# Kernel tuning notes

Measured on AMD Instinct MI355X. Metric: run time of the kernel, lower is better.

## Reference

```python
import jax, jax.numpy as jnp
import numpy as np

POS_RATIO = 0.5
EPS = 1e-6


def setup_inputs() -> dict:
    key = jax.random.key(0)
    k1, k2, k3, k4 = jax.random.split(key, 4)
    N, C, D, H, W = 8, 256, 8, 16, 16
    q = jax.random.normal(k1, (N, C, D, H, W), dtype=jnp.float32)
    k = jax.random.normal(k2, (N, C, D, H, W), dtype=jnp.float32)
    # coords: (x0, y0, z0, x1, y1, z1) with lower-right > upper-left
    uq = jax.random.uniform(k3, (N, 3), dtype=jnp.float32) * 0.5
    uk = jax.random.uniform(k4, (N, 3), dtype=jnp.float32) * 0.5
    coord_q = jnp.concatenate([uq, uq + 0.5], axis=1)
    coord_k = jnp.concatenate([uk, uk + 0.5], axis=1)
    return {"q": q, "k": k, "coord_q": coord_q, "coord_k": coord_k}


def _centers(coord, D, H, W):
    """Per-batch voxel-center coordinates. coord: [N,6]. Returns cx, cy, cz each [N, D*H*W], plus bin diag [N]."""
    bw = (coord[:, 3] - coord[:, 0]) / W  # [N]
    bh = (coord[:, 4] - coord[:, 1]) / H
    bd = (coord[:, 5] - coord[:, 2]) / D
    gz, gy, gx = jnp.meshgrid(jnp.arange(D, dtype=coord.dtype),
                              jnp.arange(H, dtype=coord.dtype),
                              jnp.arange(W, dtype=coord.dtype), indexing="ij")
    gx = (gx + 0.5).reshape(-1)[None, :]  # [1, DHW]
    gy = (gy + 0.5).reshape(-1)[None, :]
    gz = (gz + 0.5).reshape(-1)[None, :]
    cx = gx * bw[:, None] + coord[:, 0][:, None]
    cy = gy * bh[:, None] + coord[:, 1][:, None]
    cz = gz * bd[:, None] + coord[:, 2][:, None]
    diag = jnp.sqrt(bw ** 2 + bh ** 2 + bd ** 2)  # [N]
    return cx, cy, cz, diag


def reference(q, k, coord_q, coord_k):
    N, C, D, H, W = q.shape
    qf = q.reshape(N, C, -1)  # [N, C, P], P = D*H*W
    kf = k.reshape(N, C, -1)
    cqx, cqy, cqz, q_diag = _centers(coord_q, D, H, W)
    ckx, cky, ckz, k_diag = _centers(coord_k, D, H, W)
    max_diag = jnp.maximum(q_diag, k_diag)  # [N]
    # pairwise center distance, normalized by max bin diagonal: [N, P, P]
    dist = jnp.sqrt((cqx[:, :, None] - ckx[:, None, :]) ** 2
                    + (cqy[:, :, None] - cky[:, None, :]) ** 2
                    + (cqz[:, :, None] - ckz[:, None, :]) ** 2) / max_diag[:, None, None]
    pos_mask = jax.lax.stop_gradient((dist < POS_RATIO).astype(q.dtype))
    # logit[n, p, p'] = sum_c q[n,c,p] * k[n,c,p']
    logit = jnp.einsum("ncp,ncq->npq", qf, kf)
    loss = (logit * pos_mask).sum((-2, -1)) / (pos_mask.sum((-2, -1)) + EPS)  # [N]
    return -2.0 * loss.mean()
```

## Files before the change

### kernel.cpp

```cpp
#include <hip/hip_runtime.h>
#include <cstdint>
#include <cstddef>

#define NB 8
#define CH 256
#define DD 8
#define HH 16
#define WW 16
#define PP 2048

#define OFF_DPART 16384

__device__ __forceinline__ int z_window(float czq, float bdk, float k2, float maxd) {
    float lim = 0.500060f * maxd;
    int zk0 = -1;
    #pragma unroll
    for (int zk = 0; zk < DD; ++zk) {
        float czk = __fadd_rn(__fmul_rn(__fadd_rn((float)zk, 0.5f), bdk), k2);
        bool feas = fabsf(__fsub_rn(czq, czk)) < lim;
        if (feas && zk0 < 0) zk0 = zk;
    }
    if (zk0 > DD - 2) zk0 = DD - 2;
    return zk0;
}

#define CC 16
__global__ __launch_bounds__(256) void fused_kernel(
    const float* __restrict__ q, const float* __restrict__ k,
    const float* __restrict__ coord_q, const float* __restrict__ coord_k,
    float* __restrict__ partial, float* __restrict__ dpart)
{
    __shared__ float klds[CC][512];

    int t  = threadIdx.x;
    int wv = t >> 6;
    int lane = t & 63;
    int cg = blockIdx.x;
    int zq = blockIdx.y;
    int n  = blockIdx.z;
    int flat = (n * 8 + zq) * 16 + cg;
    int c0 = cg * CC;

    const float* cq = coord_q + n * 6;
    const float* ck = coord_k + n * 6;
    float q0 = cq[0], q1 = cq[1], q2 = cq[2];
    float k0 = ck[0], k1 = ck[1], k2 = ck[2];
    float bwq = __fdiv_rn(__fsub_rn(cq[3], q0), (float)WW);
    float bhq = __fdiv_rn(__fsub_rn(cq[4], q1), (float)HH);
    float bdq = __fdiv_rn(__fsub_rn(cq[5], q2), (float)DD);
    float bwk = __fdiv_rn(__fsub_rn(ck[3], k0), (float)WW);
    float bhk = __fdiv_rn(__fsub_rn(ck[4], k1), (float)HH);
    float bdk = __fdiv_rn(__fsub_rn(ck[5], k2), (float)DD);
    float diagq = __fsqrt_rn(__fadd_rn(__fadd_rn(__fmul_rn(bwq, bwq), __fmul_rn(bhq, bhq)),
                                       __fmul_rn(bdq, bdq)));
    float diagk = __fsqrt_rn(__fadd_rn(__fadd_rn(__fmul_rn(bwk, bwk), __fmul_rn(bhk, bhk)),
                                       __fmul_rn(bdk, bdk)));
    float maxd = fmaxf(diagq, diagk);
    float cqz = __fadd_rn(__fmul_rn(__fadd_rn((float)zq, 0.5f), bdq), q2);

    int zk0 = z_window(cqz, bdk, k2, maxd);
    if (zk0 < 0) {
        if (lane == 0) {
            partial[flat * 4 + wv] = 0.0f;
            if (cg == 0) dpart[(n * 8 + zq) * 4 + wv] = 0.0f;
        }
        return;
    }
    int base_p = zk0 << 8;

    int p = (zq << 8) + t;
    float qv[CC];
    {
        const float* qcol = q + ((size_t)(n * CH + c0)) * PP + p;
        #pragma unroll
        for (int c = 0; c < CC; ++c)
            qv[c] = qcol[(size_t)c * PP];
    }

    {
        const float* ksrc = k + ((size_t)(n * CH + c0)) * PP + base_p;
        #pragma unroll
        for (int i = 0; i < 8; ++i) {
            int f = i * 256 + t;
            int c = f >> 7;
            int u = (f & 127) << 2;
            float4 v = *(const float4*)(ksrc + (size_t)c * PP + u);
            klds[c][u + 0] = v.x;
            klds[c][u + 1] = v.y;
            klds[c][u + 2] = v.z;
            klds[c][u + 3] = v.w;
        }
    }
    __syncthreads();

    int ix = t & 15, iy = (t >> 4) & 15;
    float cqx = __fadd_rn(__fmul_rn(__fadd_rn((float)ix, 0.5f), bwq), q0);
    float cqy = __fadd_rn(__fmul_rn(__fadd_rn((float)iy, 0.5f), bhq), q1);

    float lim = 0.500060f * maxd;
    float tx = (cqx - k0) / bwk - 0.5f;
    float ty = (cqy - k1) / bhk - 0.5f;
    float rx = lim / bwk + 0.03f;
    float ry = lim / bhk + 0.03f;
    int jx0 = (int)ceilf(tx - rx);  if (jx0 < 0) jx0 = 0;
    int jx1 = (int)floorf(tx + rx); if (jx1 > WW - 1) jx1 = WW - 1;
    int jy0 = (int)ceilf(ty - ry);  if (jy0 < 0) jy0 = 0;
    int jy1 = (int)floorf(ty + ry); if (jy1 > HH - 1) jy1 = HH - 1;

    float half_maxd = 0.5f * maxd;
    float thr2 = half_maxd * half_maxd * 1.001f;

    float s[CC];
    #pragma unroll
    for (int c = 0; c < CC; ++c) s[c] = 0.0f;
    int cnt = 0;

    for (int dzI = 0; dzI < 2; ++dzI) {
        int jz = zk0 + dzI;
        float ckz = __fadd_rn(__fmul_rn(__fadd_rn((float)jz, 0.5f), bdk), k2);
        float dz  = __fsub_rn(cqz, ckz);
        float dz2 = __fmul_rn(dz, dz);
        for (int jy = jy0; jy <= jy1; ++jy) {
            float cky = __fadd_rn(__fmul_rn(__fadd_rn((float)jy, 0.5f), bhk), k1);
            float dy  = __fsub_rn(cqy, cky);
            float dy2 = __fmul_rn(dy, dy);
            for (int jx = jx0; jx <= jx1; ++jx) {
                float ckx = __fadd_rn(__fmul_rn(__fadd_rn((float)jx, 0.5f), bwk), k0);
                float dx  = __fsub_rn(cqx, ckx);
                float dx2 = __fmul_rn(dx, dx);
                float d2  = __fadd_rn(__fadd_rn(dx2, dy2), dz2);
                bool pos = false;
                if (d2 < thr2) {
                    float dist = __fdiv_rn(__fsqrt_rn(d2), maxd);
                    pos = dist < 0.5f;
                }
                if (pos) {
                    ++cnt;
                    int idx = (dzI << 8) + (jy << 4) + jx;
                    #pragma unroll
                    for (int c = 0; c < CC; ++c)
                        s[c] += klds[c][idx];
                }
            }
        }
    }

    float acc = 0.0f;
    #pragma unroll
    for (int c = 0; c < CC; ++c)
        acc += qv[c] * s[c];

    int ci = cnt;
    #pragma unroll
    for (int off = 32; off > 0; off >>= 1) {
        acc += __shfl_down(acc, off, 64);
        ci  += __shfl_down(ci, off, 64);
    }
    if (lane == 0) {
        partial[flat * 4 + wv] = acc;
        if (cg == 0) dpart[(n * 8 + zq) * 4 + wv] = (float)ci;
    }
}

__global__ __launch_bounds__(512) void final_kernel(const float* __restrict__ partial,
                                                    const float* __restrict__ dpart,
                                                    float* __restrict__ out)
{
    __shared__ float numsh[NB];
    __shared__ float densh[NB];
    int t = threadIdx.x;
    int n = t >> 6, lane = t & 63;

    float sp = 0.0f;
    #pragma unroll
    for (int i = 0; i < 8; ++i)
        sp += partial[n * 512 + i * 64 + lane];
    float sc = (lane < 32) ? dpart[n * 32 + lane] : 0.0f;
    #pragma unroll
    for (int off = 32; off > 0; off >>= 1) {
        sp += __shfl_down(sp, off, 64);
        sc += __shfl_down(sc, off, 64);
    }
    if (lane == 0) { numsh[n] = sp; densh[n] = sc; }
    __syncthreads();
    if (t == 0) {
        float r = 0.0f;
        for (int i = 0; i < NB; ++i)
            r += numsh[i] / (densh[i] + 1e-6f);
        out[0] = -2.0f * (r / (float)NB);
    }
}

extern "C" void kernel_launch(void* const* d_in, const int* in_sizes, int n_in,
                              void* d_out, int out_size, void* d_ws, size_t ws_size,
                              hipStream_t stream) {
    const float* q       = (const float*)d_in[0];
    const float* k       = (const float*)d_in[1];
    const float* coord_q = (const float*)d_in[2];
    const float* coord_k = (const float*)d_in[3];
    float* out = (float*)d_out;

    char* w = (char*)d_ws;
    float* partial = (float*)w;
    float* dpart   = (float*)(w + OFF_DPART);

    fused_kernel<<<dim3(CH / CC, DD, NB), 256, 0, stream>>>(q, k, coord_q, coord_k,
                                                            partial, dpart);
    final_kernel<<<1, 512, 0, stream>>>(partial, dpart, out);
}
```

Before: 80.80 us.

## Fuse final reduction via last-block counter and load K directly to LDS

Removes the separate final reduction kernel: every block increments a global atomic counter, and the last block reads all partials and writes the output. K tiles are now copied with global_load_lds straight into shared memory, and a z slice is loaded only when it is feasible. This removes one kernel launch and the register round-trip for K, but adds a memset on the stream plus atomic and fence overhead.

```diff
diff --git a/kernel.cpp b/kernel.cpp
--- a/kernel.cpp
+++ b/kernel.cpp
@@ -10,6 +10,8 @@
 #define PP 2048
 
 #define OFF_DPART 16384
+#define OFF_CTR   17408
+#define NBLK      1024
 
 __device__ __forceinline__ int z_window(float czq, float bdk, float k2, float maxd) {
     float lim = 0.500060f * maxd;
@@ -24,13 +26,20 @@
     return zk0;
 }
 
+typedef __attribute__((address_space(3))) void       lds_void;
+typedef __attribute__((address_space(1))) const void glb_void;
+
 #define CC 16
 __global__ __launch_bounds__(256) void fused_kernel(
     const float* __restrict__ q, const float* __restrict__ k,
     const float* __restrict__ coord_q, const float* __restrict__ coord_k,
-    float* __restrict__ partial, float* __restrict__ dpart)
+    float* __restrict__ partial, float* __restrict__ dpart,
+    unsigned* __restrict__ counter, float* __restrict__ out)
 {
     __shared__ float klds[CC][512];
+    __shared__ float numsh[NB];
+    __shared__ float densh[NB];
+    __shared__ int   is_last;
 
     int t  = threadIdx.x;
     int wv = t >> 6;
@@ -59,96 +68,110 @@
     float cqz = __fadd_rn(__fmul_rn(__fadd_rn((float)zq, 0.5f), bdq), q2);
 
     int zk0 = z_window(cqz, bdk, k2, maxd);
-    if (zk0 < 0) {
-        if (lane == 0) {
-            partial[flat * 4 + wv] = 0.0f;
-            if (cg == 0) dpart[(n * 8 + zq) * 4 + wv] = 0.0f;
-        }
-        return;
-    }
-    int base_p = zk0 << 8;
-
-    int p = (zq << 8) + t;
-    float qv[CC];
-    {
-        const float* qcol = q + ((size_t)(n * CH + c0)) * PP + p;
+
+    float acc = 0.0f;
+    int cnt = 0;
+
+    if (zk0 >= 0) {
+        float lim = 0.500060f * maxd;
+
+        float czk0 = __fadd_rn(__fmul_rn(__fadd_rn((float)zk0, 0.5f), bdk), k2);
+        float czk1 = __fadd_rn(__fmul_rn(__fadd_rn((float)(zk0 + 1), 0.5f), bdk), k2);
+        bool feas0 = fabsf(__fsub_rn(cqz, czk0)) < lim;
+        bool feas1 = fabsf(__fsub_rn(cqz, czk1)) < lim;
+
+        {
+            int u = (t & 63) << 2;
+            if (feas0) {
+                const float* ksrc = k + ((size_t)(n * CH + c0)) * PP + (zk0 << 8);
+                #pragma unroll
+                for (int i = 0; i < 4; ++i) {
+                    int c = i * 4 + wv;
+                    const float* src = ksrc + (size_t)c * PP + u;
+                    float* dst = &klds[c][u];
+                    __builtin_amdgcn_global_load_lds((const glb_void*)src,
+                                                     (lds_void*)dst, 16, 0, 0);
+                }
+            }
+            if (feas1) {
+                const float* ksrc = k + ((size_t)(n * CH + c0)) * PP + ((zk0 + 1) << 8);
+                #pragma unroll
+                for (int i = 0; i < 4; ++i) {
+                    int c = i * 4 + wv;
+                    const float* src = ksrc + (size_t)c * PP + u;
+                    float* dst = &klds[c][256 + u];
+                    __builtin_amdgcn_global_load_lds((const glb_void*)src,
+                                                     (lds_void*)dst, 16, 0, 0);
+                }
+            }
+        }
+
+        int p = (zq << 8) + t;
+        float qv[CC];
+        {
+            const float* qcol = q + ((size_t)(n * CH + c0)) * PP + p;
+            #pragma unroll
+            for (int c = 0; c < CC; ++c)
+                qv[c] = qcol[(size_t)c * PP];
+        }
+
+        int ix = t & 15, iy = (t >> 4) & 15;
+        float cqx = __fadd_rn(__fmul_rn(__fadd_rn((float)ix, 0.5f), bwq), q0);
+        float cqy = __fadd_rn(__fmul_rn(__fadd_rn((float)iy, 0.5f), bhq), q1);
+
+        float tx = (cqx - k0) / bwk - 0.5f;
+        float ty = (cqy - k1) / bhk - 0.5f;
+        float rx = lim / bwk + 0.03f;
+        float ry = lim / bhk + 0.03f;
+        int jx0 = (int)ceilf(tx - rx);  if (jx0 < 0) jx0 = 0;
+        int jx1 = (int)floorf(tx + rx); if (jx1 > WW - 1) jx1 = WW - 1;
+        int jy0 = (int)ceilf(ty - ry);  if (jy0 < 0) jy0 = 0;
+        int jy1 = (int)floorf(ty + ry); if (jy1 > HH - 1) jy1 = HH - 1;
+
+        float half_maxd = 0.5f * maxd;
+        float thr2 = half_maxd * half_maxd * 1.001f;
+
+        float s[CC];
+        #pragma unroll
+        for (int c = 0; c < CC; ++c) s[c] = 0.0f;
+
+        __syncthreads();
+
+        for (int dzI = 0; dzI < 2; ++dzI) {
+            if (dzI == 0 ? !feas0 : !feas1) continue;
+            int jz = zk0 + dzI;
+            float ckz = __fadd_rn(__fmul_rn(__fadd_rn((float)jz, 0.5f), bdk), k2);
+            float dz  = __fsub_rn(cqz, ckz);
+            float dz2 = __fmul_rn(dz, dz);
+            for (int jy = jy0; jy <= jy1; ++jy) {
+                float cky = __fadd_rn(__fmul_rn(__fadd_rn((float)jy, 0.5f), bhk), k1);
+                float dy  = __fsub_rn(cqy, cky);
+                float dy2 = __fmul_rn(dy, dy);
+                for (int jx = jx0; jx <= jx1; ++jx) {
+                    float ckx = __fadd_rn(__fmul_rn(__fadd_rn((float)jx, 0.5f), bwk), k0);
+                    float dx  = __fsub_rn(cqx, ckx);
+                    float dx2 = __fmul_rn(dx, dx);
+                    float d2  = __fadd_rn(__fadd_rn(dx2, dy2), dz2);
+                    bool pos = false;
+                    if (d2 < thr2) {
+                        float dist = __fdiv_rn(__fsqrt_rn(d2), maxd);
+                        pos = dist < 0.5f;
+                    }
+                    if (pos) {
+                        ++cnt;
+                        int idx = (dzI << 8) + (jy << 4) + jx;
+                        #pragma unroll
+                        for (int c = 0; c < CC; ++c)
+                            s[c] += klds[c][idx];
+                    }
+                }
+            }
+        }
+
         #pragma unroll
         for (int c = 0; c < CC; ++c)
-            qv[c] = qcol[(size_t)c * PP];
-    }
-
-    {
-        const float* ksrc = k + ((size_t)(n * CH + c0)) * PP + base_p;
-        #pragma unroll
-        for (int i = 0; i < 8; ++i) {
-            int f = i * 256 + t;
-            int c = f >> 7;
-            int u = (f & 127) << 2;
-            float4 v = *(const float4*)(ksrc + (size_t)c * PP + u);
-            klds[c][u + 0] = v.x;
-            klds[c][u + 1] = v.y;
-            klds[c][u + 2] = v.z;
-            klds[c][u + 3] = v.w;
-        }
-    }
-    __syncthreads();
-
-    int ix = t & 15, iy = (t >> 4) & 15;
-    float cqx = __fadd_rn(__fmul_rn(__fadd_rn((float)ix, 0.5f), bwq), q0);
-    float cqy = __fadd_rn(__fmul_rn(__fadd_rn((float)iy, 0.5f), bhq), q1);
-
-    float lim = 0.500060f * maxd;
-    float tx = (cqx - k0) / bwk - 0.5f;
-    float ty = (cqy - k1) / bhk - 0.5f;
-    float rx = lim / bwk + 0.03f;
-    float ry = lim / bhk + 0.03f;
-    int jx0 = (int)ceilf(tx - rx);  if (jx0 < 0) jx0 = 0;
-    int jx1 = (int)floorf(tx + rx); if (jx1 > WW - 1) jx1 = WW - 1;
-    int jy0 = (int)ceilf(ty - ry);  if (jy0 < 0) jy0 = 0;
-    int jy1 = (int)floorf(ty + ry); if (jy1 > HH - 1) jy1 = HH - 1;
-
-    float half_maxd = 0.5f * maxd;
-    float thr2 = half_maxd * half_maxd * 1.001f;
-
-    float s[CC];
-    #pragma unroll
-    for (int c = 0; c < CC; ++c) s[c] = 0.0f;
-    int cnt = 0;
-
-    for (int dzI = 0; dzI < 2; ++dzI) {
-        int jz = zk0 + dzI;
-        float ckz = __fadd_rn(__fmul_rn(__fadd_rn((float)jz, 0.5f), bdk), k2);
-        float dz  = __fsub_rn(cqz, ckz);
-        float dz2 = __fmul_rn(dz, dz);
-        for (int jy = jy0; jy <= jy1; ++jy) {
-            float cky = __fadd_rn(__fmul_rn(__fadd_rn((float)jy, 0.5f), bhk), k1);
-            float dy  = __fsub_rn(cqy, cky);
-            float dy2 = __fmul_rn(dy, dy);
-            for (int jx = jx0; jx <= jx1; ++jx) {
-                float ckx = __fadd_rn(__fmul_rn(__fadd_rn((float)jx, 0.5f), bwk), k0);
-                float dx  = __fsub_rn(cqx, ckx);
-                float dx2 = __fmul_rn(dx, dx);
-                float d2  = __fadd_rn(__fadd_rn(dx2, dy2), dz2);
-                bool pos = false;
-                if (d2 < thr2) {
-                    float dist = __fdiv_rn(__fsqrt_rn(d2), maxd);
-                    pos = dist < 0.5f;
-                }
-                if (pos) {
-                    ++cnt;
-                    int idx = (dzI << 8) + (jy << 4) + jx;
-                    #pragma unroll
-                    for (int c = 0; c < CC; ++c)
-                        s[c] += klds[c][idx];
-                }
-            }
-        }
-    }
-
-    float acc = 0.0f;
-    #pragma unroll
-    for (int c = 0; c < CC; ++c)
-        acc += qv[c] * s[c];
+            acc += qv[c] * s[c];
+    }
 
     int ci = cnt;
     #pragma unroll
@@ -157,37 +180,49 @@
         ci  += __shfl_down(ci, off, 64);
     }
     if (lane == 0) {
-        partial[flat * 4 + wv] = acc;
-        if (cg == 0) dpart[(n * 8 + zq) * 4 + wv] = (float)ci;
-    }
-}
-
-__global__ __launch_bounds__(512) void final_kernel(const float* __restrict__ partial,
-                                                    const float* __restrict__ dpart,
-                                                    float* __restrict__ out)
-{
-    __shared__ float numsh[NB];
-    __shared__ float densh[NB];
-    int t = threadIdx.x;
-    int n = t >> 6, lane = t & 63;
-
-    float sp = 0.0f;
-    #pragma unroll
-    for (int i = 0; i < 8; ++i)
-        sp += partial[n * 512 + i * 64 + lane];
-    float sc = (lane < 32) ? dpart[n * 32 + lane] : 0.0f;
-    #pragma unroll
-    for (int off = 32; off > 0; off >>= 1) {
-        sp += __shfl_down(sp, off, 64);
-        sc += __shfl_down(sc, off, 64);
-    }
-    if (lane == 0) { numsh[n] = sp; densh[n] = sc; }
+        __hip_atomic_store(&partial[flat * 4 + wv], acc,
+                           __ATOMIC_RELAXED, __HIP_MEMORY_SCOPE_AGENT);
+        if (cg == 0)
+            __hip_atomic_store(&dpart[(n * 8 + zq) * 4 + wv], (float)ci,
+                               __ATOMIC_RELAXED, __HIP_MEMORY_SCOPE_AGENT);
+    }
     __syncthreads();
+
     if (t == 0) {
-        float r = 0.0f;
-        for (int i = 0; i < NB; ++i)
-            r += numsh[i] / (densh[i] + 1e-6f);
-        out[0] = -2.0f * (r / (float)NB);
+        __threadfence();
+        unsigned old = __hip_atomic_fetch_add(counter, 1u,
+                                              __ATOMIC_ACQ_REL, __HIP_MEMORY_SCOPE_AGENT);
+        is_last = (old == NBLK - 1) ? 1 : 0;
+    }
+    __syncthreads();
+
+    if (is_last) {
+        #pragma unroll
+        for (int rep = 0; rep < 2; ++rep) {
+            int nn = wv + rep * 4;
+            float sp = 0.0f;
+            #pragma unroll
+            for (int i = 0; i < 8; ++i)
+                sp += __hip_atomic_load(&partial[nn * 512 + i * 64 + lane],
+                                        __ATOMIC_RELAXED, __HIP_MEMORY_SCOPE_AGENT);
+            float sc = (lane < 32)
+                ? __hip_atomic_load(&dpart[nn * 32 + lane],
+                                    __ATOMIC_RELAXED, __HIP_MEMORY_SCOPE_AGENT)
+                : 0.0f;
+            #pragma unroll
+            for (int off = 32; off > 0; off >>= 1) {
+                sp += __shfl_down(sp, off, 64);
+                sc += __shfl_down(sc, off, 64);
+            }
+            if (lane == 0) { numsh[nn] = sp; densh[nn] = sc; }
+        }
+        __syncthreads();
+        if (t == 0) {
+            float r = 0.0f;
+            for (int i = 0; i < NB; ++i)
+                r += numsh[i] / (densh[i] + 1e-6f);
+            out[0] = -2.0f * (r / (float)NB);
+        }
     }
 }
 
@@ -201,10 +236,12 @@
     float* out = (float*)d_out;
 
     char* w = (char*)d_ws;
-    float* partial = (float*)w;
-    float* dpart   = (float*)(w + OFF_DPART);
-
-    fused_kernel<<<dim3(CH / CC, DD, NB), 256, 0, stream>>>(q, k, coord_q, coord_k,
-                                                            partial, dpart);
-    final_kernel<<<1, 512, 0, stream>>>(partial, dpart, out);
+    float*    partial = (float*)w;
+    float*    dpart   = (float*)(w + OFF_DPART);
+    unsigned* counter = (unsigned*)(w + OFF_CTR);
+
+    hipMemsetAsync((void*)counter, 0, sizeof(unsigned), stream);
+
+    fused_kernel<<<dim3(CH / CC, DD, NB), 256, 0, stream>>>(
+        q, k, coord_q, coord_k, partial, dpart, counter, out);
 }
```

Result: slower. 126.9 us (+57.1%).

## Load K slices directly to LDS asynchronously and skip infeasible z-planes

Applied to the files above, without the earlier changes.

Replaces the register-staged float4 K copy into shared memory with global_load_lds direct-to-LDS transfers, and issues them before the Q column loads and window setup so the copies overlap that work. Each of the two candidate K z-planes is now loaded and scanned only if it passes the z-feasibility test, which removes unnecessary traffic and loop iterations. This relies on the amdgcn direct-to-LDS builtin and its wave-uniform addressing and layout assumptions, and keeps the synchronisation ordering unchanged.

```diff
diff --git a/kernel.cpp b/kernel.cpp
--- a/kernel.cpp
+++ b/kernel.cpp
@@ -23,6 +23,9 @@
     if (zk0 > DD - 2) zk0 = DD - 2;
     return zk0;
 }
+
+typedef __attribute__((address_space(3))) void       lds_void;
+typedef __attribute__((address_space(1))) const void glb_void;
 
 #define CC 16
 __global__ __launch_bounds__(256) void fused_kernel(
@@ -59,96 +62,110 @@
     float cqz = __fadd_rn(__fmul_rn(__fadd_rn((float)zq, 0.5f), bdq), q2);
 
     int zk0 = z_window(cqz, bdk, k2, maxd);
-    if (zk0 < 0) {
-        if (lane == 0) {
-            partial[flat * 4 + wv] = 0.0f;
-            if (cg == 0) dpart[(n * 8 + zq) * 4 + wv] = 0.0f;
-        }
-        return;
-    }
-    int base_p = zk0 << 8;
-
-    int p = (zq << 8) + t;
-    float qv[CC];
-    {
-        const float* qcol = q + ((size_t)(n * CH + c0)) * PP + p;
-        #pragma unroll
-        for (int c = 0; c < CC; ++c)
-            qv[c] = qcol[(size_t)c * PP];
-    }
-
-    {
-        const float* ksrc = k + ((size_t)(n * CH + c0)) * PP + base_p;
-        #pragma unroll
-        for (int i = 0; i < 8; ++i) {
-            int f = i * 256 + t;
-            int c = f >> 7;
-            int u = (f & 127) << 2;
-            float4 v = *(const float4*)(ksrc + (size_t)c * PP + u);
-            klds[c][u + 0] = v.x;
-            klds[c][u + 1] = v.y;
-            klds[c][u + 2] = v.z;
-            klds[c][u + 3] = v.w;
-        }
-    }
-    __syncthreads();
-
-    int ix = t & 15, iy = (t >> 4) & 15;
-    float cqx = __fadd_rn(__fmul_rn(__fadd_rn((float)ix, 0.5f), bwq), q0);
-    float cqy = __fadd_rn(__fmul_rn(__fadd_rn((float)iy, 0.5f), bhq), q1);
-
-    float lim = 0.500060f * maxd;
-    float tx = (cqx - k0) / bwk - 0.5f;
-    float ty = (cqy - k1) / bhk - 0.5f;
-    float rx = lim / bwk + 0.03f;
-    float ry = lim / bhk + 0.03f;
-    int jx0 = (int)ceilf(tx - rx);  if (jx0 < 0) jx0 = 0;
-    int jx1 = (int)floorf(tx + rx); if (jx1 > WW - 1) jx1 = WW - 1;
-    int jy0 = (int)ceilf(ty - ry);  if (jy0 < 0) jy0 = 0;
-    int jy1 = (int)floorf(ty + ry); if (jy1 > HH - 1) jy1 = HH - 1;
-
-    float half_maxd = 0.5f * maxd;
-    float thr2 = half_maxd * half_maxd * 1.001f;
-
-    float s[CC];
-    #pragma unroll
-    for (int c = 0; c < CC; ++c) s[c] = 0.0f;
+
+    float acc = 0.0f;
     int cnt = 0;
 
-    for (int dzI = 0; dzI < 2; ++dzI) {
-        int jz = zk0 + dzI;
-        float ckz = __fadd_rn(__fmul_rn(__fadd_rn((float)jz, 0.5f), bdk), k2);
-        float dz  = __fsub_rn(cqz, ckz);
-        float dz2 = __fmul_rn(dz, dz);
-        for (int jy = jy0; jy <= jy1; ++jy) {
-            float cky = __fadd_rn(__fmul_rn(__fadd_rn((float)jy, 0.5f), bhk), k1);
-            float dy  = __fsub_rn(cqy, cky);
-            float dy2 = __fmul_rn(dy, dy);
-            for (int jx = jx0; jx <= jx1; ++jx) {
-                float ckx = __fadd_rn(__fmul_rn(__fadd_rn((float)jx, 0.5f), bwk), k0);
-                float dx  = __fsub_rn(cqx, ckx);
-                float dx2 = __fmul_rn(dx, dx);
-                float d2  = __fadd_rn(__fadd_rn(dx2, dy2), dz2);
-                bool pos = false;
-                if (d2 < thr2) {
-                    float dist = __fdiv_rn(__fsqrt_rn(d2), maxd);
-                    pos = dist < 0.5f;
+    if (zk0 >= 0) {
+        float lim = 0.500060f * maxd;
+
+        float czk0 = __fadd_rn(__fmul_rn(__fadd_rn((float)zk0, 0.5f), bdk), k2);
+        float czk1 = __fadd_rn(__fmul_rn(__fadd_rn((float)(zk0 + 1), 0.5f), bdk), k2);
+        bool feas0 = fabsf(__fsub_rn(cqz, czk0)) < lim;
+        bool feas1 = fabsf(__fsub_rn(cqz, czk1)) < lim;
+
+        {
+            int u = (t & 63) << 2;
+            if (feas0) {
+                const float* ksrc = k + ((size_t)(n * CH + c0)) * PP + (zk0 << 8);
+                #pragma unroll
+                for (int i = 0; i < 4; ++i) {
+                    int c = i * 4 + wv;
+                    const float* src = ksrc + (size_t)c * PP + u;
+                    float* dst = &klds[c][u];
+                    __builtin_amdgcn_global_load_lds((const glb_void*)src,
+                                                     (lds_void*)dst, 16, 0, 0);
                 }
-                if (pos) {
-                    ++cnt;
-                    int idx = (dzI << 8) + (jy << 4) + jx;
-                    #pragma unroll
-                    for (int c = 0; c < CC; ++c)
-                        s[c] += klds[c][idx];
+            }
+            if (feas1) {
+                const float* ksrc = k + ((size_t)(n * CH + c0)) * PP + ((zk0 + 1) << 8);
+                #pragma unroll
+                for (int i = 0; i < 4; ++i) {
+                    int c = i * 4 + wv;
+                    const float* src = ksrc + (size_t)c * PP + u;
+                    float* dst = &klds[c][256 + u];
+                    __builtin_amdgcn_global_load_lds((const glb_void*)src,
+                                                     (lds_void*)dst, 16, 0, 0);
                 }
             }
         }
-    }
-
-    float acc = 0.0f;
-    #pragma unroll
-    for (int c = 0; c < CC; ++c)
-        acc += qv[c] * s[c];
+
+        int p = (zq << 8) + t;
+        float qv[CC];
+        {
+            const float* qcol = q + ((size_t)(n * CH + c0)) * PP + p;
+            #pragma unroll
+            for (int c = 0; c < CC; ++c)
+                qv[c] = qcol[(size_t)c * PP];
+        }
+
+        int ix = t & 15, iy = (t >> 4) & 15;
+        float cqx = __fadd_rn(__fmul_rn(__fadd_rn((float)ix, 0.5f), bwq), q0);
+        float cqy = __fadd_rn(__fmul_rn(__fadd_rn((float)iy, 0.5f), bhq), q1);
+
+        float tx = (cqx - k0) / bwk - 0.5f;
+        float ty = (cqy - k1) / bhk - 0.5f;
+        float rx = lim / bwk + 0.03f;
+        float ry = lim / bhk + 0.03f;
+        int jx0 = (int)ceilf(tx - rx);  if (jx0 < 0) jx0 = 0;
+        int jx1 = (int)floorf(tx + rx); if (jx1 > WW - 1) jx1 = WW - 1;
+        int jy0 = (int)ceilf(ty - ry);  if (jy0 < 0) jy0 = 0;
+        int jy1 = (int)floorf(ty + ry); if (jy1 > HH - 1) jy1 = HH - 1;
+
+        float half_maxd = 0.5f * maxd;
+        float thr2 = half_maxd * half_maxd * 1.001f;
+
+        float s[CC];
+        #pragma unroll
+        for (int c = 0; c < CC; ++c) s[c] = 0.0f;
+
+        __syncthreads();
+
+        for (int dzI = 0; dzI < 2; ++dzI) {
+            if (dzI == 0 ? !feas0 : !feas1) continue;
+            int jz = zk0 + dzI;
+            float ckz = __fadd_rn(__fmul_rn(__fadd_rn((float)jz, 0.5f), bdk), k2);
+            float dz  = __fsub_rn(cqz, ckz);
+            float dz2 = __fmul_rn(dz, dz);
+            for (int jy = jy0; jy <= jy1; ++jy) {
+                float cky = __fadd_rn(__fmul_rn(__fadd_rn((float)jy, 0.5f), bhk), k1);
+                float dy  = __fsub_rn(cqy, cky);
+                float dy2 = __fmul_rn(dy, dy);
+                for (int jx = jx0; jx <= jx1; ++jx) {
+                    float ckx = __fadd_rn(__fmul_rn(__fadd_rn((float)jx, 0.5f), bwk), k0);
+                    float dx  = __fsub_rn(cqx, ckx);
+                    float dx2 = __fmul_rn(dx, dx);
+                    float d2  = __fadd_rn(__fadd_rn(dx2, dy2), dz2);
+                    bool pos = false;
+                    if (d2 < thr2) {
+                        float dist = __fdiv_rn(__fsqrt_rn(d2), maxd);
+                        pos = dist < 0.5f;
+                    }
+                    if (pos) {
+                        ++cnt;
+                        int idx = (dzI << 8) + (jy << 4) + jx;
+                        #pragma unroll
+                        for (int c = 0; c < CC; ++c)
+                            s[c] += klds[c][idx];
+                    }
+                }
+            }
+        }
+
+        #pragma unroll
+        for (int c = 0; c < CC; ++c)
+            acc += qv[c] * s[c];
+    }
 
     int ci = cnt;
     #pragma unroll
```

Result: no change. 80.56 us (-0.3%).
